# Optimization experiments

Measured on AMD Instinct MI355X. Metric: run time of the kernel, lower is better.

## Reference

```python
import jax, jax.numpy as jnp
import numpy as np

N = 100000
E = 1600000
D_IN, D_HID, D_OUT = 128, 128, 128


def gcn_conv(x, edge_index, W, b):
    """PyG GCNConv with default symmetric normalization and added self-loops.
    out = D^{-1/2} (A + I) D^{-1/2} (x W) + b, edge weights = 1.
    """
    n = x.shape[0]
    h = x @ W                                   # [N, D_out]
    src, dst = edge_index[0], edge_index[1]     # messages flow src -> dst
    ones = jnp.ones(src.shape[0], dtype=x.dtype)
    # degree includes the self-loop (+1), computed on the target index as in PyG
    deg = jax.ops.segment_sum(ones, dst, num_segments=n) + 1.0  # [N]
    dinv = jax.lax.rsqrt(deg)                   # deg >= 1 so safe
    norm = dinv[src] * dinv[dst]                # [E]
    msg = h[src] * norm[:, None]                # [E, D_out]
    agg = jax.ops.segment_sum(msg, dst, num_segments=n)
    # self-loop contribution: norm = dinv_i * dinv_i = 1/deg_i
    out = agg + h * (dinv * dinv)[:, None] + b
    return out


def layer_norm(x, gamma, beta, eps=1e-5):
    mu = jnp.mean(x, axis=-1, keepdims=True)
    var = jnp.mean(jnp.square(x - mu), axis=-1, keepdims=True)
    return (x - mu) * jax.lax.rsqrt(var + eps) * gamma + beta


def setup_inputs() -> dict:
    key = jax.random.key(0)
    ks = jax.random.split(key, 8)
    x = jax.random.normal(ks[0], (N, D_IN), dtype=jnp.float32)
    edge_index = jax.random.randint(ks[1], (2, E), 0, N, dtype=jnp.int64)
    s1 = 1.0 / np.sqrt(D_IN)
    s2 = 1.0 / np.sqrt(D_HID)
    W1 = jax.random.uniform(ks[2], (D_IN, D_HID), jnp.float32, -s1, s1)
    b1 = jnp.zeros((D_HID,), jnp.float32)
    W2 = jax.random.uniform(ks[3], (D_HID, D_OUT), jnp.float32, -s2, s2)
    b2 = jnp.zeros((D_OUT,), jnp.float32)
    gamma = jnp.ones((D_OUT,), jnp.float32)
    beta = jnp.zeros((D_OUT,), jnp.float32)
    return {"x": x, "edge_index": edge_index, "W1": W1, "b1": b1,
            "W2": W2, "b2": b2, "gamma": gamma, "beta": beta}


def reference(x, edge_index, W1, b1, W2, b2, gamma, beta):
    h = gcn_conv(x, edge_index, W1, b1)
    h = jax.nn.relu(h)
    # dropout is identity in eval mode (deterministic reference)
    h = gcn_conv(h, edge_index, W2, b2)
    return layer_norm(h, gamma, beta)
```

## Files before the change

kernel.cpp:

```cpp
#include <hip/hip_runtime.h>


#define N_NODES 100000
#define N_EDGES 1600000
#define NBLK_N  391
#define NB      391
#define BKT_CAP 4736
#define BIN_GRID 391
#define GEMM_GRID 1563

typedef unsigned int  u32;
typedef unsigned short u16;
typedef unsigned char u8;
typedef unsigned long long u64;
typedef __attribute__((ext_vector_type(8))) short bf16x8;
typedef __attribute__((ext_vector_type(4))) float f32x4;

__device__ __forceinline__ float bflo(u32 u){ return __uint_as_float(u << 16); }
__device__ __forceinline__ float bfhi(u32 u){ return __uint_as_float(u & 0xFFFF0000u); }
__device__ __forceinline__ u32 f2b(float f){
  u32 u = __float_as_uint(f);
  return (u + 0x7FFFu + ((u >> 16) & 1u)) >> 16;
}
__device__ __forceinline__ u32 pack2(float a, float b){ return f2b(a) | (f2b(b) << 16); }
__device__ __forceinline__ u32 clampN(int s){
  u32 u = (u32)s;
  return (u < (u32)N_NODES) ? u : (u32)(N_NODES - 1);
}

__global__ __launch_bounds__(64) void detect(const int* __restrict__ ei,
                                             int* __restrict__ flags){
  int l = threadIdx.x;
  int nzodd = (ei[2 * l + 1] != 0) ? 1 : 0;
  #pragma unroll
  for (int o = 32; o > 0; o >>= 1) nzodd += __shfl_xor(nzodd, o, 64);
  if (l == 0) flags[1] = (nzodd == 0) ? 1 : 0;
}


__device__ __forceinline__ void prep_body(const float* __restrict__ W,
                                          u16* __restrict__ dst, int tid){
  #pragma unroll
  for (int i = 0; i < 8; ++i){
    int fid   = tid + i * 256;
    int lane  = fid & 63;
    int kb    = (fid >> 6) & 3;
    int ntile = fid >> 8;
    int n  = ntile * 16 + (lane & 15);
    int k0 = kb * 32 + (lane >> 4) * 8;
    u16 tmp[8];
    #pragma unroll
    for (int j = 0; j < 8; ++j) tmp[j] = (u16)f2b(W[(k0 + j) * 128 + n]);
    *(bf16x8*)(dst + (size_t)fid * 8) = *(const bf16x8*)tmp;
  }
}

__global__ __launch_bounds__(256) void prep_frags(const float* __restrict__ W1,
                                                  const float* __restrict__ W2,
                                                  u16* __restrict__ w1f,
                                                  u16* __restrict__ w2f){
  prep_body(blockIdx.x ? W2 : W1, blockIdx.x ? w2f : w1f, threadIdx.x);
}


__device__ __forceinline__ void gemm_tail(const u16* __restrict__ wfrag,
                                          const bf16x8 afrag[4],
                                          int rowbase, int lane,
                                          u16* __restrict__ Hout, int nrows){
  const int m = lane & 15, q = lane >> 4;
  f32x4 acc[8];
  #pragma unroll
  for (int n = 0; n < 8; ++n) acc[n] = (f32x4){0.f, 0.f, 0.f, 0.f};
  #pragma unroll
  for (int n = 0; n < 8; ++n){
    #pragma unroll
    for (int kb = 0; kb < 4; ++kb){
      bf16x8 bfrag = *(const bf16x8*)(wfrag + ((size_t)(n * 4 + kb) * 64 + lane) * 8);
      acc[n] = __builtin_amdgcn_mfma_f32_16x16x32_bf16(afrag[kb], bfrag, acc[n], 0, 0, 0);
    }
  }
  #pragma unroll
  for (int r = 0; r < 4; ++r){
    int orow = rowbase + q * 4 + r;
    if (orow < nrows){
      u16* Or = Hout + (size_t)orow * 128 + m;
      #pragma unroll
      for (int n = 0; n < 8; ++n) Or[n * 16] = (u16)f2b(acc[n][r]);
    }
  }
}

__device__ __forceinline__ void gemm_f32_body(const u16* __restrict__ wfragG,
                                              const float* __restrict__ A,
                                              u16* __restrict__ Hout, int nrows, int bid){
  const int lane = threadIdx.x & 63;
  const int wv   = threadIdx.x >> 6;
  const int rowbase = bid * 64 + wv * 16;
  const int row  = rowbase + (lane & 15);
  const int rowc = (row < nrows) ? row : (nrows - 1);
  const int q    = lane >> 4;
  bf16x8 afrag[4];
  const float* Ar = A + (size_t)rowc * 128;
  #pragma unroll
  for (int kb = 0; kb < 4; ++kb){
    f32x4 p0 = *(const f32x4*)(Ar + kb * 32 + q * 8);
    f32x4 p1 = *(const f32x4*)(Ar + kb * 32 + q * 8 + 4);
    bf16x8 f;
    f[0] = (short)f2b(p0[0]); f[1] = (short)f2b(p0[1]);
    f[2] = (short)f2b(p0[2]); f[3] = (short)f2b(p0[3]);
    f[4] = (short)f2b(p1[0]); f[5] = (short)f2b(p1[1]);
    f[6] = (short)f2b(p1[2]); f[7] = (short)f2b(p1[3]);
    afrag[kb] = f;
  }
  gemm_tail(wfragG, afrag, rowbase, lane, Hout, nrows);
}

__device__ __forceinline__ void gemm_bf16_body(const u16* __restrict__ wfragG,
                                               const u16* __restrict__ A,
                                               u16* __restrict__ Hout, int nrows, int bid){
  const int lane = threadIdx.x & 63;
  const int wv   = threadIdx.x >> 6;
  const int rowbase = bid * 64 + wv * 16;
  const int row  = rowbase + (lane & 15);
  const int rowc = (row < nrows) ? row : (nrows - 1);
  const int q    = lane >> 4;
  bf16x8 afrag[4];
  const u16* Ar = A + (size_t)rowc * 128;
  #pragma unroll
  for (int kb = 0; kb < 4; ++kb)
    afrag[kb] = *(const bf16x8*)(Ar + kb * 32 + q * 8);
  gemm_tail(wfragG, afrag, rowbase, lane, Hout, nrows);
}


__device__ __forceinline__ void binA_body(u32* smem ,
                                          const int* __restrict__ ei,
                                          u32* __restrict__ binned,
                                          u32* __restrict__ bucket_fill, int bb){
  u32* cnt   = smem;
  u32* gbase = smem + NB;
  u32* flagp = smem + 2 * NB;
  const int tid = threadIdx.x;
  for (int i = tid; i < NB; i += 256) cnt[i] = 0;
  if (tid < 64){
    int nz = (ei[2 * tid + 1] != 0) ? 1 : 0;
    u64 b = __ballot(nz);
    if (tid == 0) *flagp = (b == 0ull) ? 1u : 0u;
  }
  __syncthreads();
  const int i64  = (int)*flagp;
  const int base = bb * 4096;
  u32 pk[16], rk[16], bk[16];
  #pragma unroll
  for (int j = 0; j < 16; ++j){
    int e = base + tid + j * 256;
    bk[j] = 0xFFFFFFFFu;
    if (e < N_EDGES){
      int dsti = i64 ? ei[2 * N_EDGES + 2 * e] : ei[N_EDGES + e];
      int srci = i64 ? ei[2 * e]               : ei[e];
      u32 ud = clampN(dsti), us = clampN(srci);
      u32 b = ud >> 8;
      bk[j] = b;
      pk[j] = us | ((ud & 255u) << 17);
      rk[j] = atomicAdd(&cnt[b], 1u);
    }
  }
  __syncthreads();
  for (int i = tid; i < NB; i += 256){
    u32 c = cnt[i];
    gbase[i] = c ? atomicAdd(&bucket_fill[i], c) : 0u;
  }
  __syncthreads();
  #pragma unroll
  for (int j = 0; j < 16; ++j){
    if (bk[j] != 0xFFFFFFFFu){
      u32 idx = gbase[bk[j]] + rk[j];
      if (idx < BKT_CAP) binned[(size_t)bk[j] * BKT_CAP + idx] = pk[j];
    }
  }
}


__global__ __launch_bounds__(256) void bin_prep(const int* __restrict__ ei,
                                                u32* __restrict__ binned,
                                                u32* __restrict__ bucket_fill,
                                                const float* __restrict__ W1,
                                                const float* __restrict__ W2,
                                                u16* __restrict__ w1f,
                                                u16* __restrict__ w2f){
  __shared__ u32 smem[2 * NB + 1];
  if (blockIdx.x < BIN_GRID){
    binA_body(smem, ei, binned, bucket_fill, blockIdx.x);
  } else {
    int pb = blockIdx.x - BIN_GRID;
    prep_body(pb ? W2 : W1, pb ? w2f : w1f, threadIdx.x);
  }
}


__device__ __forceinline__ void fill_sort_body(u32* smem ,
                                               const u32* __restrict__ binned,
                                               const u32* __restrict__ bucket_fill,
                                               int* __restrict__ offs,
                                               float* __restrict__ dinv,
                                               int* __restrict__ srclist, int b){
  u32* cnt = smem;
  u32* sc  = smem + 256;
  u32* red = smem + 512;
  const int tid = threadIdx.x;
  cnt[tid] = 0;

  u32 v = 0;
  for (int i = tid; i < b; i += 256){
    u32 f = bucket_fill[i];
    v += (f > BKT_CAP) ? BKT_CAP : f;
  }
  red[tid] = v;
  __syncthreads();
  for (int o = 128; o > 0; o >>= 1){
    if (tid < o) red[tid] += red[tid + o];
    __syncthreads();
  }
  const u32 base = red[0];

  u32 n = bucket_fill[b]; if (n > BKT_CAP) n = BKT_CAP;
  const u32* eb = binned + (size_t)b * BKT_CAP;

  for (u32 i = tid; i < n; i += 256)
    atomicAdd(&cnt[eb[i] >> 17], 1u);
  __syncthreads();

  u32 own = cnt[tid];
  sc[tid] = own;
  __syncthreads();
  for (int o = 1; o < 256; o <<= 1){
    u32 add = (tid >= o) ? sc[tid - o] : 0;
    __syncthreads();
    sc[tid] += add;
    __syncthreads();
  }
  u32 pex = sc[tid] - own;

  const u32 node = ((u32)b << 8) + tid;
  if (node < (u32)N_NODES){
    offs[node] = (int)(base + pex);
    dinv[node] = rsqrtf((float)own + 1.0f);
  }
  if (b == NB - 1 && tid == 0) offs[N_NODES] = (int)(base + n);

  __syncthreads();
  sc[tid]  = pex;
  cnt[tid] = 0;
  __syncthreads();

  for (u32 i = tid; i < n; i += 256){
    u32 pk = eb[i];
    u32 d  = pk >> 17;
    u32 r  = atomicAdd(&cnt[d], 1u);
    srclist[base + sc[d] + r] = (int)(pk & 0x1FFFFu);
  }
}


__global__ __launch_bounds__(256) void fused_fs_gemm(const u32* __restrict__ binned,
                                                     const u32* __restrict__ bucket_fill,
                                                     int* __restrict__ offs,
                                                     float* __restrict__ dinv,
                                                     int* __restrict__ srclist,
                                                     const float* __restrict__ A,
                                                     const u16* __restrict__ w1frag,
                                                     u16* __restrict__ Hout){
  __shared__ u32 smem[768];
  if (blockIdx.x < NB){
    fill_sort_body(smem, binned, bucket_fill, offs, dinv, srclist, blockIdx.x);
  } else {
    gemm_f32_body(w1frag, A, Hout, N_NODES, blockIdx.x - NB);
  }
}

__global__ __launch_bounds__(256) void gemm_f32in(const float* __restrict__ A,
                                                  const u16* __restrict__ wfragG,
                                                  u16* __restrict__ Hout){
  gemm_f32_body(wfragG, A, Hout, N_NODES, blockIdx.x);
}
__global__ __launch_bounds__(256) void gemm_bf16in(const u16* __restrict__ A,
                                                   const u16* __restrict__ wfragG,
                                                   u16* __restrict__ Hout){
  gemm_bf16_body(wfragG, A, Hout, N_NODES, blockIdx.x);
}


__global__ __launch_bounds__(256) void count_deg(const int* __restrict__ ei,
                                                 const int* __restrict__ flags,
                                                 int* __restrict__ deg){
  int e   = blockIdx.x * 256 + threadIdx.x;
  int i64 = flags[1];
  int dst = i64 ? ei[2 * N_EDGES + 2 * e] : ei[N_EDGES + e];
  if ((unsigned)dst < (unsigned)N_NODES) atomicAdd(&deg[dst], 1);
}

__global__ __launch_bounds__(256) void fill_edges(const int* __restrict__ ei,
                                                  const int* __restrict__ flags,
                                                  int* __restrict__ woff,
                                                  int* __restrict__ srclist){
  int e   = blockIdx.x * 256 + threadIdx.x;
  int i64 = flags[1];
  int dst = i64 ? ei[2 * N_EDGES + 2 * e] : ei[N_EDGES + e];
  int src = i64 ? ei[2 * e]               : ei[e];
  if ((unsigned)dst < (unsigned)N_NODES){
    int p = atomicAdd(&woff[dst], 1);
    if ((unsigned)p < (unsigned)N_EDGES) srclist[p] = clampN(src);
  }
}

__global__ __launch_bounds__(256) void scan1(const int* __restrict__ deg,
                                             int* __restrict__ offs,
                                             int* __restrict__ bsum,
                                             float* __restrict__ dinv){
  __shared__ int sh[256];
  int t = threadIdx.x;
  int i = blockIdx.x * 256 + t;
  int v = (i < N_NODES) ? deg[i] : 0;
  if (i < N_NODES) dinv[i] = rsqrtf((float)v + 1.0f);
  sh[t] = v;
  __syncthreads();
  for (int o = 1; o < 256; o <<= 1){
    int add = (t >= o) ? sh[t - o] : 0;
    __syncthreads();
    sh[t] += add;
    __syncthreads();
  }
  if (i < N_NODES) offs[i] = sh[t] - v;
  if (t == 255)    bsum[blockIdx.x] = sh[255];
}

__global__ __launch_bounds__(512) void scan2(const int* __restrict__ bsum,
                                             int* __restrict__ bofs){
  __shared__ int sh[512];
  int t = threadIdx.x;
  int v = (t < NBLK_N) ? bsum[t] : 0;
  sh[t] = v;
  __syncthreads();
  for (int o = 1; o < 512; o <<= 1){
    int add = (t >= o) ? sh[t - o] : 0;
    __syncthreads();
    sh[t] += add;
    __syncthreads();
  }
  if (t < NBLK_N) bofs[t] = sh[t] - v;
}

__global__ __launch_bounds__(256) void finalize_offs(int* __restrict__ offs,
                                                     const int* __restrict__ bofs,
                                                     int* __restrict__ woff){
  int i = blockIdx.x * 256 + threadIdx.x;
  if (i < N_NODES){
    int o = offs[i] + bofs[blockIdx.x];
    offs[i] = o;
    woff[i] = o;
  }
  if (i == 0) offs[N_NODES] = N_EDGES;
}


#define GATHER_EDGE(sv, A0, A1)                         \
  { u32 s_ = (u32)(sv);                                 \
    float w_ = dinv[s_];                                \
    u32 h_ = H[s_ * 64 + lane];                         \
    A0 = fmaf(w_, bflo(h_), A0);                        \
    A1 = fmaf(w_, bfhi(h_), A1); }

#define GATHER_BODY                                     \
  int beg = offs[node], end = offs[node + 1];           \
  if (end > N_EDGES) end = N_EDGES;                     \
  if (beg < 0 || beg > end) beg = end;                  \
  float a0 = 0.f, a1 = 0.f, c0 = 0.f, c1 = 0.f;         \
  int e = beg;                                          \
  for (; e + 8 <= end; e += 8){                         \
    int s0=srcl[e],s1=srcl[e+1],s2=srcl[e+2],s3=srcl[e+3]; \
    int s4=srcl[e+4],s5=srcl[e+5],s6=srcl[e+6],s7=srcl[e+7]; \
    GATHER_EDGE(s0,a0,a1) GATHER_EDGE(s1,c0,c1)         \
    GATHER_EDGE(s2,a0,a1) GATHER_EDGE(s3,c0,c1)         \
    GATHER_EDGE(s4,a0,a1) GATHER_EDGE(s5,c0,c1)         \
    GATHER_EDGE(s6,a0,a1) GATHER_EDGE(s7,c0,c1)         \
  }                                                     \
  for (; e + 4 <= end; e += 4){                         \
    int s0=srcl[e],s1=srcl[e+1],s2=srcl[e+2],s3=srcl[e+3]; \
    GATHER_EDGE(s0,a0,a1) GATHER_EDGE(s1,c0,c1)         \
    GATHER_EDGE(s2,a0,a1) GATHER_EDGE(s3,c0,c1)         \
  }                                                     \
  for (; e < end; ++e){ int s0=srcl[e]; GATHER_EDGE(s0,a0,a1) } \
  a0 += c0;  a1 += c1;                                  \
  float di = dinv[node];                                \
  u32 hs = H[(u32)node * 64 + lane];                    \
  float v0 = fmaf(a0, di, fmaf(bflo(hs), di * di, bb0)); \
  float v1 = fmaf(a1, di, fmaf(bfhi(hs), di * di, bb1));

__global__ __launch_bounds__(256) void gather_relu(const int* __restrict__ offs,
                                                   const int* __restrict__ srcl,
                                                   const u32* __restrict__ H,
                                                   const float* __restrict__ dinv,
                                                   const float* __restrict__ bias,
                                                   u32* __restrict__ X2){
  const int node = blockIdx.x * 4 + (threadIdx.x >> 6);
  const int lane = threadIdx.x & 63;
  const float bb0 = bias[2 * lane], bb1 = bias[2 * lane + 1];
  GATHER_BODY
  X2[(u32)node * 64 + lane] = pack2(fmaxf(v0, 0.f), fmaxf(v1, 0.f));
}

__global__ __launch_bounds__(256) void gather_ln(const int* __restrict__ offs,
                                                 const int* __restrict__ srcl,
                                                 const u32* __restrict__ H,
                                                 const float* __restrict__ dinv,
                                                 const float* __restrict__ bias,
                                                 const float* __restrict__ gamma,
                                                 const float* __restrict__ beta,
                                                 float* __restrict__ out){
  const int node = blockIdx.x * 4 + (threadIdx.x >> 6);
  const int lane = threadIdx.x & 63;
  const float bb0 = bias[2 * lane], bb1 = bias[2 * lane + 1];
  GATHER_BODY

  float s2 = v0 + v1;
  #pragma unroll
  for (int o = 32; o > 0; o >>= 1) s2 += __shfl_xor(s2, o, 64);
  float mu = s2 * 0.0078125f;
  float d0 = v0 - mu, d1 = v1 - mu;
  float qq = d0 * d0 + d1 * d1;
  #pragma unroll
  for (int o = 32; o > 0; o >>= 1) qq += __shfl_xor(qq, o, 64);
  float rr = rsqrtf(qq * 0.0078125f + 1e-5f);

  float g0 = gamma[2 * lane], g1 = gamma[2 * lane + 1];
  float t0 = beta[2 * lane],  t1 = beta[2 * lane + 1];
  *(float2*)(out + (size_t)node * 128 + 2 * lane) =
      make_float2(fmaf(d0 * rr, g0, t0), fmaf(d1 * rr, g1, t1));
}


extern "C" void kernel_launch(void* const* d_in, const int* in_sizes, int n_in,
                              void* d_out, int out_size, void* d_ws, size_t ws_size,
                              hipStream_t stream){
  const float* x  = (const float*)d_in[0];
  const int*   ei = (const int*)d_in[1];
  const float* W1 = (const float*)d_in[2];
  const float* b1 = (const float*)d_in[3];
  const float* W2 = (const float*)d_in[4];
  const float* b2 = (const float*)d_in[5];
  const float* gm = (const float*)d_in[6];
  const float* bt = (const float*)d_in[7];

  char* ws = (char*)d_ws;
  size_t off = 0;
  auto carve = [&](size_t bytes) -> void* {
    void* p = ws + off;
    off = (off + bytes + 255) & ~(size_t)255;
    return p;
  };
  int*   flags       = (int*)  carve(64);
  u16*   w1frag      = (u16*)  carve(128 * 128 * 2);
  u16*   w2frag      = (u16*)  carve(128 * 128 * 2);
  u32*   bucket_fill = (u32*)  carve(NB * 4);
  int*   offs        = (int*)  carve((size_t)(N_NODES + 1) * 4);
  float* dinv        = (float*)carve((size_t)N_NODES * 4);
  int*   srclist     = (int*)  carve((size_t)N_EDGES * 4);
  int*   deg         = (int*)  carve((size_t)N_NODES * 4);
  int*   bsum        = (int*)  carve(2048);
  int*   bofs        = (int*)  carve(2048);

  size_t bin_bytes = (size_t)NB * BKT_CAP * 4;
  u32* binned = (u32*)carve(bin_bytes);
  bool use_binned = (ws_size >= off);
  if (!use_binned) off = (size_t)((char*)binned - ws);

  size_t h_bytes = (size_t)N_NODES * 128 * 2;
  u32* H1 = (u32*)d_out;
  u32* X2 = (u32*)d_out + 6400000;
  u32* H2 = (ws_size >= off + h_bytes) ? (u32*)carve(h_bytes) : (u32*)d_in[0];

  if (use_binned){
    hipMemsetAsync(bucket_fill, 0, NB * 4, stream);
    bin_prep      <<<BIN_GRID + 2, 256, 0, stream>>>(ei, binned, bucket_fill,
                                                     W1, W2, w1frag, w2frag);
    fused_fs_gemm <<<NB + GEMM_GRID, 256, 0, stream>>>(binned, bucket_fill, offs, dinv,
                                                       srclist, x, w1frag, (u16*)H1);
  } else {
    prep_frags    <<<2,             256, 0, stream>>>(W1, W2, w1frag, w2frag);
    hipMemsetAsync(deg, 0, (size_t)N_NODES * 4, stream);
    detect        <<<1,             64,  0, stream>>>(ei, flags);
    count_deg     <<<N_EDGES / 256, 256, 0, stream>>>(ei, flags, deg);
    scan1         <<<NBLK_N,        256, 0, stream>>>(deg, offs, bsum, dinv);
    scan2         <<<1,             512, 0, stream>>>(bsum, bofs);
    finalize_offs <<<NBLK_N,        256, 0, stream>>>(offs, bofs, deg );
    fill_edges    <<<N_EDGES / 256, 256, 0, stream>>>(ei, flags, deg , srclist);
    gemm_f32in    <<<GEMM_GRID,     256, 0, stream>>>(x, w1frag, (u16*)H1);
  }

  gather_relu <<<N_NODES / 4, 256, 0, stream>>>(offs, srclist, H1, dinv, b1, X2);
  gemm_bf16in <<<GEMM_GRID,   256, 0, stream>>>((const u16*)X2, w2frag, (u16*)H2);
  gather_ln   <<<N_NODES / 4, 256, 0, stream>>>(offs, srclist, H2, dinv, b2, gm, bt,
                                                (float*)d_out);
}
```

Baseline: 307.5 us.

## Fuse layer-1 gather/ReLU with layer-2 GEMM via shared-memory tile

Merges the first aggregation+ReLU kernel with the second bf16 GEMM. Each 64-thread block gathers 16 nodes sequentially into LDS, then runs MFMA against the W2 fragments and writes H2 directly. This removes the X2 intermediate round trip through global memory and one kernel launch. In exchange the gather runs with one wave per block and serialized node loops, which reduces memory-level parallelism and occupancy for the latency-bound gather.

```diff
diff --git a/kernel.cpp b/kernel.cpp
--- a/kernel.cpp
+++ b/kernel.cpp
@@ -8,6 +8,7 @@
 #define BKT_CAP 4736
 #define BIN_GRID 391
 #define GEMM_GRID 1563
+#define MM_GRID 6250
 
 typedef unsigned int  u32;
 typedef unsigned short u16;
@@ -112,23 +113,6 @@
     f[6] = (short)f2b(p1[2]); f[7] = (short)f2b(p1[3]);
     afrag[kb] = f;
   }
-  gemm_tail(wfragG, afrag, rowbase, lane, Hout, nrows);
-}
-
-__device__ __forceinline__ void gemm_bf16_body(const u16* __restrict__ wfragG,
-                                               const u16* __restrict__ A,
-                                               u16* __restrict__ Hout, int nrows, int bid){
-  const int lane = threadIdx.x & 63;
-  const int wv   = threadIdx.x >> 6;
-  const int rowbase = bid * 64 + wv * 16;
-  const int row  = rowbase + (lane & 15);
-  const int rowc = (row < nrows) ? row : (nrows - 1);
-  const int q    = lane >> 4;
-  bf16x8 afrag[4];
-  const u16* Ar = A + (size_t)rowc * 128;
-  #pragma unroll
-  for (int kb = 0; kb < 4; ++kb)
-    afrag[kb] = *(const bf16x8*)(Ar + kb * 32 + q * 8);
   gemm_tail(wfragG, afrag, rowbase, lane, Hout, nrows);
 }
 
@@ -282,11 +266,6 @@
                                                   const u16* __restrict__ wfragG,
                                                   u16* __restrict__ Hout){
   gemm_f32_body(wfragG, A, Hout, N_NODES, blockIdx.x);
-}
-__global__ __launch_bounds__(256) void gemm_bf16in(const u16* __restrict__ A,
-                                                   const u16* __restrict__ wfragG,
-                                                   u16* __restrict__ Hout){
-  gemm_bf16_body(wfragG, A, Hout, N_NODES, blockIdx.x);
 }
 
 
@@ -396,18 +375,48 @@
   float v0 = fmaf(a0, di, fmaf(bflo(hs), di * di, bb0)); \
   float v1 = fmaf(a1, di, fmaf(bfhi(hs), di * di, bb1));
 
-__global__ __launch_bounds__(256) void gather_relu(const int* __restrict__ offs,
-                                                   const int* __restrict__ srcl,
-                                                   const u32* __restrict__ H,
-                                                   const float* __restrict__ dinv,
-                                                   const float* __restrict__ bias,
-                                                   u32* __restrict__ X2){
-  const int node = blockIdx.x * 4 + (threadIdx.x >> 6);
-  const int lane = threadIdx.x & 63;
+
+__global__ __launch_bounds__(64) void gather_relu_mm(const int* __restrict__ offs,
+                                                     const int* __restrict__ srcl,
+                                                     const u32* __restrict__ H,
+                                                     const float* __restrict__ dinv,
+                                                     const float* __restrict__ bias,
+                                                     const u16* __restrict__ w2frag,
+                                                     u16* __restrict__ H2){
+  __shared__ u32 xs[16 * 68];
+  const int lane = threadIdx.x;
+  const int m = lane & 15, q = lane >> 4;
+  const int nodebase = blockIdx.x * 16;
+  if (nodebase >= N_NODES) return;
   const float bb0 = bias[2 * lane], bb1 = bias[2 * lane + 1];
-  GATHER_BODY
-  X2[(u32)node * 64 + lane] = pack2(fmaxf(v0, 0.f), fmaxf(v1, 0.f));
-}
+
+  #pragma unroll 1
+  for (int j = 0; j < 16; ++j){
+    const int node = nodebase + j;
+    GATHER_BODY
+    xs[j * 68 + lane] = pack2(fmaxf(v0, 0.f), fmaxf(v1, 0.f));
+  }
+
+  bf16x8 afrag[4];
+  #pragma unroll
+  for (int kb = 0; kb < 4; ++kb)
+    afrag[kb] = *(const bf16x8*)(xs + m * 68 + kb * 16 + q * 4);
+
+  #pragma unroll
+  for (int n = 0; n < 8; ++n){
+    f32x4 acc = (f32x4){0.f, 0.f, 0.f, 0.f};
+    #pragma unroll
+    for (int kb = 0; kb < 4; ++kb){
+      bf16x8 bfrag = *(const bf16x8*)(w2frag + ((size_t)(n * 4 + kb) * 64 + lane) * 8);
+      acc = __builtin_amdgcn_mfma_f32_16x16x32_bf16(afrag[kb], bfrag, acc, 0, 0, 0);
+    }
+    const int col = n * 16 + m;
+    #pragma unroll
+    for (int r = 0; r < 4; ++r)
+      H2[(size_t)(nodebase + q * 4 + r) * 128 + col] = (u16)f2b(acc[r]);
+  }
+}
+
 
 __global__ __launch_bounds__(256) void gather_ln(const int* __restrict__ offs,
                                                  const int* __restrict__ srcl,
@@ -476,7 +485,6 @@
 
   size_t h_bytes = (size_t)N_NODES * 128 * 2;
   u32* H1 = (u32*)d_out;
-  u32* X2 = (u32*)d_out + 6400000;
   u32* H2 = (ws_size >= off + h_bytes) ? (u32*)carve(h_bytes) : (u32*)d_in[0];
 
   if (use_binned){
@@ -497,8 +505,8 @@
     gemm_f32in    <<<GEMM_GRID,     256, 0, stream>>>(x, w1frag, (u16*)H1);
   }
 
-  gather_relu <<<N_NODES / 4, 256, 0, stream>>>(offs, srclist, H1, dinv, b1, X2);
-  gemm_bf16in <<<GEMM_GRID,   256, 0, stream>>>((const u16*)X2, w2frag, (u16*)H2);
-  gather_ln   <<<N_NODES / 4, 256, 0, stream>>>(offs, srclist, H2, dinv, b2, gm, bt,
-                                                (float*)d_out);
-}
+  gather_relu_mm <<<MM_GRID,     64,  0, stream>>>(offs, srclist, H1, dinv, b1,
+                                                   w2frag, (u16*)H2);
+  gather_ln      <<<N_NODES / 4, 256, 0, stream>>>(offs, srclist, H2, dinv, b2, gm, bt,
+                                                   (float*)d_out);
+}
```

Measured after the change: 320.3 us. +4.1%, slower.
